# Optimization experiments

Measured on AMD Instinct MI355X. Metric: run time of the kernel, lower is better.

Reference implementation:

```python
import jax, jax.numpy as jnp
import numpy as np

LEVELS = 10

def _haar_edges(levels=LEVELS):
    sl, el, sr, er = [], [], [], []
    for j in range(levels):
        subdiv = 2 ** j
        width = 1.0 / subdiv
        a = np.arange(subdiv, dtype=np.float64) * width
        sl.append(a)
        el.append(a + width / 2.0)
        sr.append(a + width / 2.0)
        er.append(a + width)
    cat = lambda xs: jnp.asarray(np.concatenate(xs).astype(np.float32))
    return cat(sl), cat(el), cat(sr), cat(er)

_SL, _EL, _SR, _ER = _haar_edges()

def setup_inputs() -> dict:
    key = jax.random.key(0)
    ks = jax.random.split(key, 7)
    B, T, NB, H, F = 16, 8192, 1023, 8, 3
    s1, s2, s3 = 1.0 / np.sqrt(NB), 1.0 / np.sqrt(H), 1.0 / np.sqrt(H)
    return {
        "t": jax.random.uniform(ks[0], (B, T), dtype=jnp.float32),
        "W1": jax.random.normal(ks[1], (NB, H), dtype=jnp.float32) * s1,
        "b1": jax.random.normal(ks[2], (H,), dtype=jnp.float32) * s1,
        "W2": jax.random.normal(ks[3], (H, H), dtype=jnp.float32) * s2,
        "b2": jax.random.normal(ks[4], (H,), dtype=jnp.float32) * s2,
        "W3": jax.random.normal(ks[5], (H, F), dtype=jnp.float32) * s3,
        "b3": jax.random.normal(ks[6], (F,), dtype=jnp.float32) * s3,
    }

def reference(t, W1, b1, W2, b2, W3, b3):
    B, T = t.shape
    tf = t.reshape(-1, 1)  # (B*T, 1)
    ml = (tf >= _SL) & (tf < _EL)  # left half of each Haar interval
    mr = (tf >= _SR) & (tf < _ER)  # right half
    H = ml.astype(jnp.float32) - mr.astype(jnp.float32)  # (B*T, 1023)
    h = jax.nn.relu(H @ W1 + b1)
    h = jax.nn.relu(h @ W2 + b2)
    out = h @ W3 + b3  # (B*T, features)
    return out.reshape(B, T, -1)
```

## Files before the change

### kernel.cpp

```cpp
#include <hip/hip_runtime.h>


__global__ __launch_bounds__(256) void haar_mlp_kernel(
    const float* __restrict__ t,
    const float* __restrict__ W1, const float* __restrict__ b1,
    const float* __restrict__ W2, const float* __restrict__ b2,
    const float* __restrict__ W3, const float* __restrict__ b3,
    float* __restrict__ out, int n)
{
    __shared__ float4 w1s[2046];
    #pragma unroll
    for (int u = 0; u < 8; ++u) {
        int idx = (int)threadIdx.x + u * 256;
        if (idx < 2046) w1s[idx] = reinterpret_cast<const float4*>(W1)[idx];
    }
    __syncthreads();

    int i = blockIdx.x * 256 + (int)threadIdx.x;
    if (i >= n) return;

    float tv = t[i];

    float h1[8];
    #pragma unroll
    for (int o = 0; o < 8; ++o) h1[o] = b1[o];

    #pragma unroll
    for (int j = 0; j < 10; ++j) {
        float tj = tv * (float)(1 << j);
        float fl = floorf(tj);
        int k = (int)fl;
        int kmax = (1 << j) - 1;
        k = (k < 0) ? 0 : (k > kmax ? kmax : k);
        float sgn = (tj - fl < 0.5f) ? 1.0f : -1.0f;
        int row = (1 << j) - 1 + k;
        float4 lo = w1s[row * 2 + 0];
        float4 hi = w1s[row * 2 + 1];
        h1[0] += sgn * lo.x; h1[1] += sgn * lo.y;
        h1[2] += sgn * lo.z; h1[3] += sgn * lo.w;
        h1[4] += sgn * hi.x; h1[5] += sgn * hi.y;
        h1[6] += sgn * hi.z; h1[7] += sgn * hi.w;
    }
    #pragma unroll
    for (int o = 0; o < 8; ++o) h1[o] = fmaxf(h1[o], 0.0f);

    float h2[8];
    #pragma unroll
    for (int o = 0; o < 8; ++o) {
        float a = b2[o];
        #pragma unroll
        for (int q = 0; q < 8; ++q) a = fmaf(h1[q], W2[q * 8 + o], a);
        h2[o] = fmaxf(a, 0.0f);
    }

    float o0 = b3[0], o1 = b3[1], o2 = b3[2];
    #pragma unroll
    for (int q = 0; q < 8; ++q) {
        o0 = fmaf(h2[q], W3[q * 3 + 0], o0);
        o1 = fmaf(h2[q], W3[q * 3 + 1], o1);
        o2 = fmaf(h2[q], W3[q * 3 + 2], o2);
    }
    out[i * 3 + 0] = o0;
    out[i * 3 + 1] = o1;
    out[i * 3 + 2] = o2;
}

extern "C" void kernel_launch(void* const* d_in, const int* in_sizes, int n_in,
                              void* d_out, int out_size, void* d_ws, size_t ws_size,
                              hipStream_t stream) {
    const float* t  = (const float*)d_in[0];
    const float* W1 = (const float*)d_in[1];
    const float* b1 = (const float*)d_in[2];
    const float* W2 = (const float*)d_in[3];
    const float* b2 = (const float*)d_in[4];
    const float* W3 = (const float*)d_in[5];
    const float* b3 = (const float*)d_in[6];
    float* out = (float*)d_out;

    int n = in_sizes[0];
    int grid = (n + 255) / 256;
    haar_mlp_kernel<<<grid, 256, 0, stream>>>(t, W1, b1, W2, b2, W3, b3, out, n);
}
```

Measured before the change: 10.21 us.

## Precompute MLP outputs per Haar bin into LUT, then gather per sample

Every t falling in the same 1/1024 bin produces the same Haar feature vector, so the full MLP output depends only on the bin index. A small first kernel evaluates the MLP for all 1024 bins into a workspace lookup table. A second kernel stages the table in shared memory and maps each sample to its bin with one gather. This removes the per-sample W1 gathers and MLP arithmetic, at the cost of an extra kernel launch and a dependency between the two kernels.

```diff
diff --git a/kernel.cpp b/kernel.cpp
--- a/kernel.cpp
+++ b/kernel.cpp
@@ -1,25 +1,14 @@
 #include <hip/hip_runtime.h>
 
 
-__global__ __launch_bounds__(256) void haar_mlp_kernel(
-    const float* __restrict__ t,
+__global__ __launch_bounds__(256) void haar_build_lut(
     const float* __restrict__ W1, const float* __restrict__ b1,
     const float* __restrict__ W2, const float* __restrict__ b2,
     const float* __restrict__ W3, const float* __restrict__ b3,
-    float* __restrict__ out, int n)
+    float4* __restrict__ lut)
 {
-    __shared__ float4 w1s[2046];
-    #pragma unroll
-    for (int u = 0; u < 8; ++u) {
-        int idx = (int)threadIdx.x + u * 256;
-        if (idx < 2046) w1s[idx] = reinterpret_cast<const float4*>(W1)[idx];
-    }
-    __syncthreads();
-
-    int i = blockIdx.x * 256 + (int)threadIdx.x;
-    if (i >= n) return;
-
-    float tv = t[i];
+    int u = blockIdx.x * 256 + (int)threadIdx.x;
+    if (u >= 1024) return;
 
     float h1[8];
     #pragma unroll
@@ -27,15 +16,11 @@
 
     #pragma unroll
     for (int j = 0; j < 10; ++j) {
-        float tj = tv * (float)(1 << j);
-        float fl = floorf(tj);
-        int k = (int)fl;
-        int kmax = (1 << j) - 1;
-        k = (k < 0) ? 0 : (k > kmax ? kmax : k);
-        float sgn = (tj - fl < 0.5f) ? 1.0f : -1.0f;
-        int row = (1 << j) - 1 + k;
-        float4 lo = w1s[row * 2 + 0];
-        float4 hi = w1s[row * 2 + 1];
+        int row = (1 << j) - 1 + (u >> (10 - j));
+        float sgn = ((u >> (9 - j)) & 1) ? -1.0f : 1.0f;
+        const float4* wp = reinterpret_cast<const float4*>(W1 + row * 8);
+        float4 lo = wp[0];
+        float4 hi = wp[1];
         h1[0] += sgn * lo.x; h1[1] += sgn * lo.y;
         h1[2] += sgn * lo.z; h1[3] += sgn * lo.w;
         h1[4] += sgn * hi.x; h1[5] += sgn * hi.y;
@@ -60,9 +45,30 @@
         o1 = fmaf(h2[q], W3[q * 3 + 1], o1);
         o2 = fmaf(h2[q], W3[q * 3 + 2], o2);
     }
-    out[i * 3 + 0] = o0;
-    out[i * 3 + 1] = o1;
-    out[i * 3 + 2] = o2;
+    lut[u] = make_float4(o0, o1, o2, 0.0f);
+}
+
+__global__ __launch_bounds__(256) void haar_apply_lut(
+    const float* __restrict__ t,
+    const float4* __restrict__ lut,
+    float* __restrict__ out, int n)
+{
+    __shared__ float4 l[1024];
+    #pragma unroll
+    for (int u = 0; u < 4; ++u)
+        l[(int)threadIdx.x + u * 256] = lut[(int)threadIdx.x + u * 256];
+    __syncthreads();
+
+    int i = blockIdx.x * 256 + (int)threadIdx.x;
+    if (i >= n) return;
+
+    float tv = t[i];
+    int u = (int)(tv * 1024.0f);
+    u = (u < 0) ? 0 : (u > 1023 ? 1023 : u);
+    float4 r = l[u];
+    out[i * 3 + 0] = r.x;
+    out[i * 3 + 1] = r.y;
+    out[i * 3 + 2] = r.z;
 }
 
 extern "C" void kernel_launch(void* const* d_in, const int* in_sizes, int n_in,
@@ -76,8 +82,9 @@
     const float* W3 = (const float*)d_in[5];
     const float* b3 = (const float*)d_in[6];
     float* out = (float*)d_out;
+    float4* lut = (float4*)d_ws;
 
     int n = in_sizes[0];
-    int grid = (n + 255) / 256;
-    haar_mlp_kernel<<<grid, 256, 0, stream>>>(t, W1, b1, W2, b2, W3, b3, out, n);
+    haar_build_lut<<<4, 256, 0, stream>>>(W1, b1, W2, b2, W3, b3, lut);
+    haar_apply_lut<<<(n + 255) / 256, 256, 0, stream>>>(t, lut, out, n);
 }
```

New measurement: 11.56 us. +13.2%, slower.
